# Kernel tuning notes

Hardware: AMD Instinct MI355X
Metric: run time of the kernel (lower is better)

Reference implementation:

```python
import jax, jax.numpy as jnp
import numpy as np

NUM_EMBEDDINGS = 1024
EMBEDDING_DIM = 256
COMMITMENT_COST = 0.25


def setup_inputs() -> dict:
    key = jax.random.key(0)
    k1, k2 = jax.random.split(key)
    z = jax.random.normal(k1, (32, 256, 32, 32), dtype=jnp.float32)
    # matches torch init: uniform(-1/K, 1/K)
    codebook = jax.random.uniform(
        k2, (NUM_EMBEDDINGS, EMBEDDING_DIM), dtype=jnp.float32,
        minval=-1.0 / NUM_EMBEDDINGS, maxval=1.0 / NUM_EMBEDDINGS)
    return {"z": z, "codebook": codebook}


def reference(z, codebook):
    B, C, H, W = z.shape
    # b c h w -> (b h w) c
    z_nhwc = jnp.transpose(z, (0, 2, 3, 1))
    zf = z_nhwc.reshape(-1, C)  # [N, D]
    # squared euclidean distances [N, K]
    d = (jnp.sum(zf * zf, axis=1, keepdims=True)
         + jnp.sum(codebook * codebook, axis=1)
         - 2.0 * zf @ codebook.T)
    indices = jnp.argmin(d, axis=1)  # [N]
    zq_nhwc = codebook[indices].reshape(B, H, W, C)
    z_q = jnp.transpose(zq_nhwc, (0, 3, 1, 2))  # [B, C, H, W]

    codebook_loss = jnp.mean((jax.lax.stop_gradient(z_q) - z) ** 2)
    commitment_loss = jnp.mean((z_q - jax.lax.stop_gradient(z)) ** 2)
    vq_loss = codebook_loss + COMMITMENT_COST * commitment_loss

    # straight-through estimator
    z_q_st = z + jax.lax.stop_gradient(z_q - z)
    indices_bhw = indices.reshape(B, H, W)
    return z_q_st, vq_loss, indices_bhw
```

## Files before the change

### kernel.cpp

```cpp
#include <hip/hip_runtime.h>

#define NUM_EMB 1024
#define EMB_DIM 256
#define BATCH   32
#define HW      1024
#define Z_ELEMS (BATCH*EMB_DIM*HW)
#define LOSS_OFF Z_ELEMS
#define IDX_OFF (Z_ELEMS+1)

#define WS_CNORM_OFF 16
#define WS_ZNORM_OFF 2048

typedef float v2f __attribute__((ext_vector_type(2)));

__global__ __launch_bounds__(256) void k_cnorm(const float* __restrict__ cb,
                                               float* __restrict__ ws) {
    int k = blockIdx.x * 256 + threadIdx.x;
    if (k == 0) ws[0] = 0.0f;
    const float* row = cb + (size_t)k * EMB_DIM;
    float half[2];
#pragma unroll
    for (int h = 0; h < 2; ++h) {
        const float* a = row + h * 128;
        float r[8];
#pragma unroll
        for (int j = 0; j < 8; ++j) r[j] = __fmul_rn(a[j], a[j]);
        for (int i = 8; i < 128; i += 8)
#pragma unroll
            for (int j = 0; j < 8; ++j)
                r[j] = __fadd_rn(r[j], __fmul_rn(a[i + j], a[i + j]));
        half[h] = __fadd_rn(__fadd_rn(__fadd_rn(r[0], r[1]), __fadd_rn(r[2], r[3])),
                            __fadd_rn(__fadd_rn(r[4], r[5]), __fadd_rn(r[6], r[7])));
    }
    ws[WS_CNORM_OFF + k] = __fadd_rn(half[0], half[1]);
}

__global__ __launch_bounds__(256) void k_znorm(const float* __restrict__ z,
                                               float* __restrict__ ws) {
    int n = blockIdx.x * 256 + threadIdx.x;
    int b = n >> 10, p = n & 1023;
    const float* base = z + (size_t)b * EMB_DIM * HW + p;
    float half[2];
#pragma unroll
    for (int h = 0; h < 2; ++h) {
        float r[8];
#pragma unroll
        for (int j = 0; j < 8; ++j) {
            float v = base[(size_t)(h * 128 + j) * HW];
            r[j] = __fmul_rn(v, v);
        }
        for (int i = 8; i < 128; i += 8)
#pragma unroll
            for (int j = 0; j < 8; ++j) {
                float v = base[(size_t)(h * 128 + i + j) * HW];
                r[j] = __fadd_rn(r[j], __fmul_rn(v, v));
            }
        half[h] = __fadd_rn(__fadd_rn(__fadd_rn(r[0], r[1]), __fadd_rn(r[2], r[3])),
                            __fadd_rn(__fadd_rn(r[4], r[5]), __fadd_rn(r[6], r[7])));
    }
    ws[WS_ZNORM_OFF + n] = __fadd_rn(half[0], half[1]);
}

#define MT 64
#define KC 256
#define DC 16
#define CPAD 260

__global__ __launch_bounds__(256, 4) void k_argmin(const float* __restrict__ z,
                                                   const float* __restrict__ cb,
                                                   const float* __restrict__ ws,
                                                   float* __restrict__ out) {
    __shared__ __attribute__((aligned(16))) float z_buf[DC * MT];
    __shared__ __attribute__((aligned(16))) float c_buf[DC * CPAD];

    const int tid = threadIdx.x;
    const int tx = tid & 15;
    const int ty = tid >> 4;
    const int b  = blockIdx.y;
    const int p0 = blockIdx.x * MT;
    const int kh = blockIdx.z;
    const int kbase = kh * 512;

    const float* zb = z + (size_t)b * EMB_DIM * HW + p0;
    const float* cn = ws + WS_CNORM_OFF;
    const float* zn = ws + WS_ZNORM_OFF + b * HW + p0;

    float z2[4];
#pragma unroll
    for (int a = 0; a < 4; ++a) z2[a] = zn[ty * 4 + a];

    float minv[4];
    int   mini[4];
#pragma unroll
    for (int a = 0; a < 4; ++a) { minv[a] = 3.402823466e+38f; mini[a] = 0; }

    const int zrow = tid >> 4;
    const int zcol = (tid & 15) << 2;

#pragma unroll 1
    for (int kc = 0; kc < 2; ++kc) {
        const int k0 = kbase + kc * KC;
        v2f acc2[4][8];
#pragma unroll
        for (int a = 0; a < 4; ++a)
#pragma unroll
            for (int j = 0; j < 8; ++j) acc2[a][j] = (v2f)(0.0f);

#pragma unroll 1
        for (int dc = 0; dc < EMB_DIM / DC; ++dc) {
            __syncthreads();
            {
                float4 v = *(const float4*)(zb + (size_t)(dc * DC + zrow) * HW + zcol);
                *(float4*)(z_buf + zrow * MT + zcol) = v;
            }
#pragma unroll
            for (int pass = 0; pass < 4; ++pass) {
                int idx = pass * 256 + tid;
                int kk  = idx >> 2;
                int seg = idx & 3;
                float4 v = *(const float4*)(cb + (size_t)(k0 + kk) * EMB_DIM + dc * DC + seg * 4);
                c_buf[(seg * 4 + 0) * CPAD + kk] = v.x;
                c_buf[(seg * 4 + 1) * CPAD + kk] = v.y;
                c_buf[(seg * 4 + 2) * CPAD + kk] = v.z;
                c_buf[(seg * 4 + 3) * CPAD + kk] = v.w;
            }
            __syncthreads();

#pragma unroll 4
            for (int d = 0; d < DC; ++d) {
                float4 za = *(const float4*)(z_buf + d * MT + ty * 4);
                float zf[4] = {za.x, za.y, za.z, za.w};
                v2f cf2[8];
#pragma unroll
                for (int j = 0; j < 4; ++j) {
                    float4 cv = *(const float4*)(c_buf + d * CPAD + j * 64 + tx * 4);
                    cf2[j * 2 + 0] = (v2f){cv.x, cv.y};
                    cf2[j * 2 + 1] = (v2f){cv.z, cv.w};
                }
#pragma unroll
                for (int a = 0; a < 4; ++a) {
                    v2f zz = (v2f){zf[a], zf[a]};
#pragma unroll
                    for (int j = 0; j < 8; ++j)
                        acc2[a][j] = __builtin_elementwise_fma(zz, cf2[j], acc2[a][j]);
                }
            }
        }
        float c2[16];
#pragma unroll
        for (int j = 0; j < 4; ++j)
#pragma unroll
            for (int c = 0; c < 4; ++c)
                c2[j * 4 + c] = cn[k0 + j * 64 + tx * 4 + c];
#pragma unroll
        for (int a = 0; a < 4; ++a) {
#pragma unroll
            for (int j = 0; j < 4; ++j) {
#pragma unroll
                for (int c = 0; c < 4; ++c) {
                    int kg = k0 + j * 64 + tx * 4 + c;
                    float dot = acc2[a][j * 2 + (c >> 1)][c & 1];
                    float t1 = __fadd_rn(z2[a], c2[j * 4 + c]);
                    float s  = __fadd_rn(t1, __fmul_rn(-2.0f, dot));
                    if (s < minv[a]) { minv[a] = s; mini[a] = kg; }
                }
            }
        }
    }

    __syncthreads();
    float* rv = c_buf;
    int*   ri = (int*)(c_buf + 1024);
#pragma unroll
    for (int a = 0; a < 4; ++a) {
        int m = ty * 4 + a;
        rv[m * 16 + tx] = minv[a];
        ri[m * 16 + tx] = mini[a];
    }
    __syncthreads();
    if (tid < MT) {
        int m = tid;
        float bv = rv[m * 16];
        int   bi = ri[m * 16];
#pragma unroll
        for (int j = 1; j < 16; ++j) {
            float v  = rv[m * 16 + j];
            int   i2 = ri[m * 16 + j];
            if (v < bv || (v == bv && i2 < bi)) { bv = v; bi = i2; }
        }
        int n = b * HW + p0 + m;
        out[2 * n + kh] = bv;
        ((int*)out)[65536 + 2 * n + kh] = bi;
    }
}

__global__ __launch_bounds__(256) void k_merge(float* __restrict__ out) {
    int n = blockIdx.x * 256 + threadIdx.x;
    float v0 = out[2 * n], v1 = out[2 * n + 1];
    const int* pi = (const int*)out + 65536;
    int i0 = pi[2 * n], i1 = pi[2 * n + 1];
    out[IDX_OFF + n] = (float)((v1 < v0) ? i1 : i0);
}

__global__ __launch_bounds__(256) void k_gather(const float* __restrict__ z,
                                                const float* __restrict__ cb,
                                                float* __restrict__ out,
                                                float* __restrict__ ws) {
    __shared__ int   s_idx[64];
    __shared__ float s_red[4];
    const int tid = threadIdx.x;
    const int b  = blockIdx.x >> 4;
    const int p0 = (blockIdx.x & 15) * 64;

    if (tid < 64)
        s_idx[tid] = (int)out[IDX_OFF + (size_t)b * HW + p0 + tid];
    __syncthreads();

    const int p = tid & 63;
    const int cbase = tid >> 6;
    const int r = s_idx[p];
    const float* zrow = z   + (size_t)b * EMB_DIM * HW + p0 + p;
    float*       orow = out + (size_t)b * EMB_DIM * HW + p0 + p;
    const float* crow = cb  + (size_t)r * EMB_DIM;

    float acc = 0.0f;
#pragma unroll 4
    for (int it = 0; it < 64; ++it) {
        int c = it * 4 + cbase;
        float zq = crow[c];
        float zv = zrow[(size_t)c * HW];
        float d  = zq - zv;
        orow[(size_t)c * HW] = zv + d;
        acc += d * d;
    }
#pragma unroll
    for (int off = 32; off > 0; off >>= 1) acc += __shfl_down(acc, off, 64);
    if ((tid & 63) == 0) s_red[tid >> 6] = acc;
    __syncthreads();
    if (tid == 0) atomicAdd(ws, s_red[0] + s_red[1] + s_red[2] + s_red[3]);
}

__global__ void k_final(const float* __restrict__ ws, float* __restrict__ out) {
    out[LOSS_OFF] = 1.25f * (ws[0] * (1.0f / 8388608.0f));
}

extern "C" void kernel_launch(void* const* d_in, const int* in_sizes, int n_in,
                              void* d_out, int out_size, void* d_ws, size_t ws_size,
                              hipStream_t stream) {
    const float* z  = (const float*)d_in[0];
    const float* cb = (const float*)d_in[1];
    float* out = (float*)d_out;
    float* ws  = (float*)d_ws;

    k_cnorm <<<NUM_EMB / 256, 256, 0, stream>>>(cb, ws);
    k_znorm <<<BATCH * HW / 256, 256, 0, stream>>>(z, ws);
    k_argmin<<<dim3(HW / MT, BATCH, 2), 256, 0, stream>>>(z, cb, ws, out);
    k_merge <<<BATCH * HW / 256, 256, 0, stream>>>(out);
    k_gather<<<BATCH * (HW / 64), 256, 0, stream>>>(z, cb, out, ws);
    k_final <<<1, 1, 0, stream>>>(ws, out);
}
```

Measured before the change: 352.4 us.

## Fuse norm kernels, merge argmin halves via packed atomicMin, inline final loss

Merges the codebook-norm and z-norm kernels into one prep launch, which also initialises a packed (distance, index) buffer. The two argmin halves now combine through a 64-bit atomicMin instead of a separate merge pass when the workspace is large enough. The gather kernel writes the indices and computes the final loss using a last-block counter, removing the k_final launch. The inner FMA loop is also rewritten with inline v_pk_fma_f32 using op_sel broadcasting, and its unroll factor changes. The intent is fewer launches and fewer VALU instructions. The packed compare relies on non-negative distances keeping float bit order, and the last-block pattern adds fence and atomic overhead.

```diff
diff --git a/kernel.cpp b/kernel.cpp
--- a/kernel.cpp
+++ b/kernel.cpp
@@ -10,55 +10,60 @@
 
 #define WS_CNORM_OFF 16
 #define WS_ZNORM_OFF 2048
+#define WS_PACKED_BYTE_OFF 262144
+#define WS_NEEDED (WS_PACKED_BYTE_OFF + 32768*8)
 
 typedef float v2f __attribute__((ext_vector_type(2)));
 
-__global__ __launch_bounds__(256) void k_cnorm(const float* __restrict__ cb,
-                                               float* __restrict__ ws) {
-    int k = blockIdx.x * 256 + threadIdx.x;
-    if (k == 0) ws[0] = 0.0f;
-    const float* row = cb + (size_t)k * EMB_DIM;
-    float half[2];
-#pragma unroll
-    for (int h = 0; h < 2; ++h) {
-        const float* a = row + h * 128;
-        float r[8];
-#pragma unroll
-        for (int j = 0; j < 8; ++j) r[j] = __fmul_rn(a[j], a[j]);
-        for (int i = 8; i < 128; i += 8)
-#pragma unroll
-            for (int j = 0; j < 8; ++j)
-                r[j] = __fadd_rn(r[j], __fmul_rn(a[i + j], a[i + j]));
-        half[h] = __fadd_rn(__fadd_rn(__fadd_rn(r[0], r[1]), __fadd_rn(r[2], r[3])),
-                            __fadd_rn(__fadd_rn(r[4], r[5]), __fadd_rn(r[6], r[7])));
-    }
-    ws[WS_CNORM_OFF + k] = __fadd_rn(half[0], half[1]);
-}
-
-__global__ __launch_bounds__(256) void k_znorm(const float* __restrict__ z,
-                                               float* __restrict__ ws) {
-    int n = blockIdx.x * 256 + threadIdx.x;
-    int b = n >> 10, p = n & 1023;
-    const float* base = z + (size_t)b * EMB_DIM * HW + p;
-    float half[2];
-#pragma unroll
-    for (int h = 0; h < 2; ++h) {
-        float r[8];
-#pragma unroll
-        for (int j = 0; j < 8; ++j) {
-            float v = base[(size_t)(h * 128 + j) * HW];
-            r[j] = __fmul_rn(v, v);
-        }
-        for (int i = 8; i < 128; i += 8)
+__global__ __launch_bounds__(256) void k_prep(const float* __restrict__ z,
+                                              const float* __restrict__ cb,
+                                              float* __restrict__ ws,
+                                              unsigned long long* __restrict__ packed) {
+    int gid = blockIdx.x * 256 + threadIdx.x;
+    if (gid == 0) { ws[0] = 0.0f; ((unsigned int*)ws)[1] = 0u; }
+    if (blockIdx.x < 4) {
+        int k = gid;
+        const float* row = cb + (size_t)k * EMB_DIM;
+        float half[2];
+#pragma unroll
+        for (int h = 0; h < 2; ++h) {
+            const float* a = row + h * 128;
+            float r[8];
+#pragma unroll
+            for (int j = 0; j < 8; ++j) r[j] = __fmul_rn(a[j], a[j]);
+            for (int i = 8; i < 128; i += 8)
+#pragma unroll
+                for (int j = 0; j < 8; ++j)
+                    r[j] = __fadd_rn(r[j], __fmul_rn(a[i + j], a[i + j]));
+            half[h] = __fadd_rn(__fadd_rn(__fadd_rn(r[0], r[1]), __fadd_rn(r[2], r[3])),
+                                __fadd_rn(__fadd_rn(r[4], r[5]), __fadd_rn(r[6], r[7])));
+        }
+        ws[WS_CNORM_OFF + k] = __fadd_rn(half[0], half[1]);
+    } else {
+        int n = gid - 1024;
+        packed[n] = 0xFFFFFFFFFFFFFFFFull;
+        int b = n >> 10, p = n & 1023;
+        const float* base = z + (size_t)b * EMB_DIM * HW + p;
+        float half[2];
+#pragma unroll
+        for (int h = 0; h < 2; ++h) {
+            float r[8];
 #pragma unroll
             for (int j = 0; j < 8; ++j) {
-                float v = base[(size_t)(h * 128 + i + j) * HW];
-                r[j] = __fadd_rn(r[j], __fmul_rn(v, v));
-            }
-        half[h] = __fadd_rn(__fadd_rn(__fadd_rn(r[0], r[1]), __fadd_rn(r[2], r[3])),
-                            __fadd_rn(__fadd_rn(r[4], r[5]), __fadd_rn(r[6], r[7])));
-    }
-    ws[WS_ZNORM_OFF + n] = __fadd_rn(half[0], half[1]);
+                float v = base[(size_t)(h * 128 + j) * HW];
+                r[j] = __fmul_rn(v, v);
+            }
+            for (int i = 8; i < 128; i += 8)
+#pragma unroll
+                for (int j = 0; j < 8; ++j) {
+                    float v = base[(size_t)(h * 128 + i + j) * HW];
+                    r[j] = __fadd_rn(r[j], __fmul_rn(v, v));
+                }
+            half[h] = __fadd_rn(__fadd_rn(__fadd_rn(r[0], r[1]), __fadd_rn(r[2], r[3])),
+                                __fadd_rn(__fadd_rn(r[4], r[5]), __fadd_rn(r[6], r[7])));
+        }
+        ws[WS_ZNORM_OFF + n] = __fadd_rn(half[0], half[1]);
+    }
 }
 
 #define MT 64
@@ -69,7 +74,7 @@
 __global__ __launch_bounds__(256, 4) void k_argmin(const float* __restrict__ z,
                                                    const float* __restrict__ cb,
                                                    const float* __restrict__ ws,
-                                                   float* __restrict__ out) {
+                                                   unsigned long long* __restrict__ packed) {
     __shared__ __attribute__((aligned(16))) float z_buf[DC * MT];
     __shared__ __attribute__((aligned(16))) float c_buf[DC * CPAD];
 
@@ -78,8 +83,7 @@
     const int ty = tid >> 4;
     const int b  = blockIdx.y;
     const int p0 = blockIdx.x * MT;
-    const int kh = blockIdx.z;
-    const int kbase = kh * 512;
+    const int kbase = blockIdx.z * 512;
 
     const float* zb = z + (size_t)b * EMB_DIM * HW + p0;
     const float* cn = ws + WS_CNORM_OFF;
@@ -126,10 +130,10 @@
             }
             __syncthreads();
 
-#pragma unroll 4
+#pragma unroll 2
             for (int d = 0; d < DC; ++d) {
-                float4 za = *(const float4*)(z_buf + d * MT + ty * 4);
-                float zf[4] = {za.x, za.y, za.z, za.w};
+                v2f za01 = *(const v2f*)(z_buf + d * MT + ty * 4);
+                v2f za23 = *(const v2f*)(z_buf + d * MT + ty * 4 + 2);
                 v2f cf2[8];
 #pragma unroll
                 for (int j = 0; j < 4; ++j) {
@@ -138,11 +142,15 @@
                     cf2[j * 2 + 1] = (v2f){cv.z, cv.w};
                 }
 #pragma unroll
-                for (int a = 0; a < 4; ++a) {
-                    v2f zz = (v2f){zf[a], zf[a]};
-#pragma unroll
-                    for (int j = 0; j < 8; ++j)
-                        acc2[a][j] = __builtin_elementwise_fma(zz, cf2[j], acc2[a][j]);
+                for (int j = 0; j < 8; ++j) {
+                    asm("v_pk_fma_f32 %0, %1, %2, %0 op_sel:[0,0,0] op_sel_hi:[0,1,1]"
+                        : "+v"(acc2[0][j]) : "v"(za01), "v"(cf2[j]));
+                    asm("v_pk_fma_f32 %0, %1, %2, %0 op_sel:[1,0,0] op_sel_hi:[1,1,1]"
+                        : "+v"(acc2[1][j]) : "v"(za01), "v"(cf2[j]));
+                    asm("v_pk_fma_f32 %0, %1, %2, %0 op_sel:[0,0,0] op_sel_hi:[0,1,1]"
+                        : "+v"(acc2[2][j]) : "v"(za23), "v"(cf2[j]));
+                    asm("v_pk_fma_f32 %0, %1, %2, %0 op_sel:[1,0,0] op_sel_hi:[1,1,1]"
+                        : "+v"(acc2[3][j]) : "v"(za23), "v"(cf2[j]));
                 }
             }
         }
@@ -189,31 +197,41 @@
             if (v < bv || (v == bv && i2 < bi)) { bv = v; bi = i2; }
         }
         int n = b * HW + p0 + m;
-        out[2 * n + kh] = bv;
-        ((int*)out)[65536 + 2 * n + kh] = bi;
-    }
-}
-
-__global__ __launch_bounds__(256) void k_merge(float* __restrict__ out) {
+        unsigned long long pk = ((unsigned long long)__float_as_uint(bv) << 32)
+                                | (unsigned long long)(unsigned)bi;
+        atomicMin(&packed[n], pk);
+    }
+}
+
+__global__ __launch_bounds__(256) void k_merge(const unsigned long long* __restrict__ packed,
+                                               float* __restrict__ out) {
     int n = blockIdx.x * 256 + threadIdx.x;
-    float v0 = out[2 * n], v1 = out[2 * n + 1];
-    const int* pi = (const int*)out + 65536;
-    int i0 = pi[2 * n], i1 = pi[2 * n + 1];
-    out[IDX_OFF + n] = (float)((v1 < v0) ? i1 : i0);
+    out[IDX_OFF + n] = (float)(int)(unsigned)(packed[n] & 0xFFFFFFFFull);
 }
 
 __global__ __launch_bounds__(256) void k_gather(const float* __restrict__ z,
                                                 const float* __restrict__ cb,
                                                 float* __restrict__ out,
-                                                float* __restrict__ ws) {
+                                                float* __restrict__ ws,
+                                                const unsigned long long* __restrict__ packed,
+                                                int fused_idx) {
     __shared__ int   s_idx[64];
     __shared__ float s_red[4];
     const int tid = threadIdx.x;
     const int b  = blockIdx.x >> 4;
     const int p0 = (blockIdx.x & 15) * 64;
 
-    if (tid < 64)
-        s_idx[tid] = (int)out[IDX_OFF + (size_t)b * HW + p0 + tid];
+    if (tid < 64) {
+        int n = b * HW + p0 + tid;
+        int bi;
+        if (fused_idx) {
+            bi = (int)(unsigned)(packed[n] & 0xFFFFFFFFull);
+            out[IDX_OFF + n] = (float)bi;
+        } else {
+            bi = (int)out[IDX_OFF + n];
+        }
+        s_idx[tid] = bi;
+    }
     __syncthreads();
 
     const int p = tid & 63;
@@ -237,11 +255,15 @@
     for (int off = 32; off > 0; off >>= 1) acc += __shfl_down(acc, off, 64);
     if ((tid & 63) == 0) s_red[tid >> 6] = acc;
     __syncthreads();
-    if (tid == 0) atomicAdd(ws, s_red[0] + s_red[1] + s_red[2] + s_red[3]);
-}
-
-__global__ void k_final(const float* __restrict__ ws, float* __restrict__ out) {
-    out[LOSS_OFF] = 1.25f * (ws[0] * (1.0f / 8388608.0f));
+    if (tid == 0) {
+        atomicAdd(ws, s_red[0] + s_red[1] + s_red[2] + s_red[3]);
+        __threadfence();
+        unsigned old = atomicAdd((unsigned int*)ws + 1, 1u);
+        if (old == 511u) {
+            float total = atomicAdd(ws, 0.0f);
+            out[LOSS_OFF] = 1.25f * (total * (1.0f / 8388608.0f));
+        }
+    }
 }
 
 extern "C" void kernel_launch(void* const* d_in, const int* in_sizes, int n_in,
@@ -252,10 +274,14 @@
     float* out = (float*)d_out;
     float* ws  = (float*)d_ws;
 
-    k_cnorm <<<NUM_EMB / 256, 256, 0, stream>>>(cb, ws);
-    k_znorm <<<BATCH * HW / 256, 256, 0, stream>>>(z, ws);
-    k_argmin<<<dim3(HW / MT, BATCH, 2), 256, 0, stream>>>(z, cb, ws, out);
-    k_merge <<<BATCH * HW / 256, 256, 0, stream>>>(out);
-    k_gather<<<BATCH * (HW / 64), 256, 0, stream>>>(z, cb, out, ws);
-    k_final <<<1, 1, 0, stream>>>(ws, out);
-}
+    const bool big_ws = (ws_size >= (size_t)WS_NEEDED);
+    unsigned long long* packed = big_ws
+        ? (unsigned long long*)((char*)d_ws + WS_PACKED_BYTE_OFF)
+        : (unsigned long long*)d_out;
+
+    k_prep  <<<132, 256, 0, stream>>>(z, cb, ws, packed);
+    k_argmin<<<dim3(HW / MT, BATCH, 2), 256, 0, stream>>>(z, cb, ws, packed);
+    if (!big_ws)
+        k_merge<<<BATCH * HW / 256, 256, 0, stream>>>(packed, out);
+    k_gather<<<BATCH * (HW / 64), 256, 0, stream>>>(z, cb, out, ws, packed, big_ws ? 1 : 0);
+}
```

New measurement: 323.5 us. 8.2% less time.
